# Kernel optimization log

Hardware: AMD Instinct MI355X
Metric: run time of the kernel (lower is better)

## Reference

```python
import jax, jax.numpy as jnp
import numpy as np

LAMBDA_L1 = 0.5
LAMBDA_SSIM = 0.5
ITERATIONS = 1000
THRESH = 0.01
SUB_N = 50000  # torch caps inlier-check set at 50k points


def setup_inputs() -> dict:
    key = jax.random.key(0)
    k1, k2 = jax.random.split(key)
    H, W = 1024, 2048  # Cityscapes resolution
    rendered_depth = jax.random.uniform(k1, (H, W), jnp.float32, 0.2, 10.0)
    prior_disparity = jax.random.uniform(k2, (H, W), jnp.float32, 0.0, 1.0)
    return {"rendered_depth": rendered_depth, "prior_disparity": prior_disparity}


def _ransac_linear_alignment(x, y, mask, key):
    """Fit y = s*x + t by RANSAC over masked points. x, y, mask are flat [P]."""
    P = x.shape[0]
    num_pts = mask.sum()
    # indices of masked points packed at the front (fixed-shape, jit-safe)
    idx_m = jnp.flatnonzero(mask, size=P, fill_value=0)
    k_pair, k_sub = jax.random.split(key)
    # random point pairs among the first num_pts (masked) entries
    pos = jax.random.randint(k_pair, (ITERATIONS, 2), 0, num_pts)
    pi = idx_m[pos]                                   # [iters, 2]
    x1, x2 = x[pi[:, 0]], x[pi[:, 1]]
    y1, y2 = y[pi[:, 0]], y[pi[:, 1]]
    scales = (y2 - y1) / (x2 - x1 + 1e-8)             # [iters]
    shifts = y1 - scales * x1                         # [iters]
    # subsample inlier-check set (with replacement; torch uses randperm)
    spos = jax.random.randint(k_sub, (SUB_N,), 0, num_pts)
    si = idx_m[spos]
    x_sub, y_sub = x[si], y[si]                       # [SUB_N]
    # dynamic threshold = 0.5 * MAD of masked y
    y_nan = jnp.where(mask, y, jnp.nan)
    med = jnp.nanmedian(y_nan)
    dyn = jnp.nanmedian(jnp.abs(y_nan - med)) * 0.5
    dyn = jnp.where(dyn < 1e-5, THRESH, dyn)
    # all iterations evaluated in parallel: [iters, SUB_N] residuals
    res = jnp.abs(scales[:, None] * x_sub[None, :] + shifts[:, None] - y_sub[None, :])
    counts = (res < dyn).sum(axis=1)
    counts = jnp.where(scales > 0, counts, -1)        # torch skips s <= 0
    best = jnp.argmax(counts)                         # first max == torch's strict-> update
    valid = counts[best] >= 0
    s = jnp.where(valid, scales[best], 1.0)
    t = jnp.where(valid, shifts[best], 0.0)
    # num_pts < 10 fallback
    s = jnp.where(num_pts < 10, 1.0, s)
    t = jnp.where(num_pts < 10, 0.0, t)
    return s, t


def reference(rendered_depth, prior_disparity):
    d_ren = rendered_depth
    d_pri = prior_disparity
    mask = (d_ren > 0.1) & (d_ren < 100.0) & jnp.isfinite(d_ren)
    target_inv_ren = 1.0 / (d_ren + 1e-6)
    n_valid = mask.sum()

    s, t = _ransac_linear_alignment(
        jax.lax.stop_gradient(d_pri).reshape(-1),
        jax.lax.stop_gradient(target_inv_ren).reshape(-1),
        mask.reshape(-1),
        jax.random.key(42),
    )
    aligned_prior_disp = s * d_pri + t
    # masked mean L1 (F.l1_loss over mask-selected elements)
    l1_loss = jnp.sum(jnp.abs(aligned_prior_disp - target_inv_ren) * mask) / jnp.maximum(n_valid, 1)
    total_loss = LAMBDA_L1 * l1_loss + LAMBDA_SSIM * 0.0  # ssim_module=None
    total_loss = jnp.where(n_valid < 100, 0.0, total_loss)  # early-exit branch
    prior_metric_depth = 1.0 / jnp.maximum(jax.lax.stop_gradient(aligned_prior_disp), 1e-4)
    return total_loss, target_inv_ren, prior_metric_depth
```

## Files before the change

kernel.cpp:

```cpp
#include <hip/hip_runtime.h>
#include <stdint.h>
#include <math.h>


#define NT 256
#define GA 128
#define GB 512
#define GC 128
#define GD 512
#define GE 256
#define GF 1024
#define LCAP 262144u

enum : uint32_t {
  W_CNT  = 0,
  W_LOSS = 4,
  W_N    = 6,
  W_VA   = 7, W_VB = 8,
  W_WA   = 9, W_WB = 10,
  W_SB1  = 12,
  W_SB2  = 16,
  W_COUNTS = 20,
  W_G1   = 1024,
  W_G2   = 17408,
  W_ZEND = 33792,
  W_PERC = 33792,
  W_SCALES = 34816,
  W_SHIFTS = 35816,
  W_XSUB = 36816,
  W_YSUB = 86816,
  W_LA1  = 136832,
  W_LB1  = W_LA1 + LCAP,
  W_LA2  = W_LB1 + LCAP,
  W_LB2  = W_LA2 + LCAP
};

__device__ __forceinline__ uint32_t rotl32(uint32_t v, int d) {
  return (v << d) | (v >> (32 - d));
}
__device__ __forceinline__ void tf2x32(uint32_t k0, uint32_t k1,
                                       uint32_t c0, uint32_t c1,
                                       uint32_t& o0, uint32_t& o1) {
  uint32_t ks2 = k0 ^ k1 ^ 0x1BD11BDAu;
  uint32_t x0 = c0 + k0;
  uint32_t x1 = c1 + k1;
#define TFR(r) { x0 += x1; x1 = rotl32(x1, r); x1 ^= x0; }
  TFR(13) TFR(15) TFR(26) TFR(6)
  x0 += k1;  x1 += ks2 + 1u;
  TFR(17) TFR(29) TFR(16) TFR(24)
  x0 += ks2; x1 += k0 + 2u;
  TFR(13) TFR(15) TFR(26) TFR(6)
  x0 += k0;  x1 += k1 + 3u;
  TFR(17) TFR(29) TFR(16) TFR(24)
  x0 += k1;  x1 += ks2 + 4u;
  TFR(13) TFR(15) TFR(26) TFR(6)
  x0 += ks2; x1 += k0 + 5u;
#undef TFR
  o0 = x0; o1 = x1;
}
struct Keys { uint32_t hp0, hp1, lp0, lp1, hs0, hs1, ls0, ls1; };
__device__ __forceinline__ Keys derive_keys() {
  Keys K; uint32_t p0, p1, q0, q1;
  tf2x32(0u, 42u, 0u, 0u, p0, p1);
  tf2x32(0u, 42u, 0u, 1u, q0, q1);
  tf2x32(p0, p1, 0u, 0u, K.hp0, K.hp1);
  tf2x32(p0, p1, 0u, 1u, K.lp0, K.lp1);
  tf2x32(q0, q1, 0u, 0u, K.hs0, K.hs1);
  tf2x32(q0, q1, 0u, 1u, K.ls0, K.ls1);
  return K;
}
__device__ __forceinline__ uint32_t bits32(uint32_t k0, uint32_t k1, uint32_t e) {
  uint32_t a, b; tf2x32(k0, k1, 0u, e, a, b); return a ^ b;
}
__device__ __forceinline__ uint32_t ri_offset(uint32_t hi, uint32_t lo, uint32_t span) {
  uint32_t m = 65536u % span;
  m = (m * m) % span;
  uint32_t off = (hi % span) * m + (lo % span);
  return off % span;
}

__device__ __forceinline__ uint32_t f2u(float f) {
  uint32_t u = __float_as_uint(f);
  return (u & 0x80000000u) ? ~u : (u | 0x80000000u);
}
__device__ __forceinline__ float u2f(uint32_t u) {
  uint32_t v = (u & 0x80000000u) ? (u & 0x7FFFFFFFu) : ~u;
  return __uint_as_float(v);
}
__device__ __forceinline__ uint32_t yval_u(float dv, float& y, bool& m) {
  y = __fdiv_rn(1.0f, __fadd_rn(dv, 1e-6f));
  m = (dv > 0.1f) && (dv < 100.0f) && isfinite(dv);
  return m ? f2u(y) : 0xFFFFFFFFu;
}
__device__ __forceinline__ uint32_t m2w(uint32_t u, float med) {
  return (u != 0xFFFFFFFFu) ? f2u(fabsf(__fsub_rn(u2f(u), med))) : 0xFFFFFFFFu;
}
__device__ __forceinline__ float med_from(const uint32_t* WS) {
  return __fmul_rn(__fadd_rn(u2f(WS[W_VA]), u2f(WS[W_VB])), 0.5f);
}

__device__ __forceinline__ uint32_t block_sum_u32(uint32_t v, uint32_t* wl) {
  const int lane = threadIdx.x & 63, wid = threadIdx.x >> 6;
  for (int off = 32; off > 0; off >>= 1) v += __shfl_down(v, off);
  __syncthreads();
  if (lane == 0) wl[wid] = v;
  __syncthreads();
  return wl[0] + wl[1] + wl[2] + wl[3];
}
__device__ __forceinline__ uint32_t scan_excl(uint32_t local, uint32_t* wl) {
  const int lane = threadIdx.x & 63, wid = threadIdx.x >> 6;
  __syncthreads();
  uint32_t v = local;
#pragma unroll
  for (int off = 1; off < 64; off <<= 1) {
    uint32_t o = __shfl_up(v, off);
    if (lane >= off) v += o;
  }
  if (lane == 63) wl[wid] = v;
  __syncthreads();
  uint32_t base = 0;
  for (int w = 0; w < 4; w++) if (w < wid) base += wl[w];
  return base + v - local;
}

__device__ void g_select2(const uint32_t* __restrict__ G, uint32_t rkA, uint32_t rkB,
                          uint32_t* wl, uint32_t* bc4) {
  const int tid = threadIdx.x;
  if (tid < 4) bc4[tid] = 0u;
  __syncthreads();
  uint32_t local = 0;
  for (int k = 0; k < 64; k++) local += G[tid * 64 + k];
  uint32_t excl = scan_excl(local, wl);
  for (int s = 0; s < 2; s++) {
    uint32_t rk = s ? rkB : rkA;
    if (local > 0 && rk >= excl && rk < excl + local) {
      uint32_t c = excl;
      for (int k = 0; k < 64; k++) {
        uint32_t v = G[tid * 64 + k];
        if (rk < c + v) { bc4[2 * s] = (uint32_t)(tid * 64 + k); bc4[2 * s + 1] = rk - c; break; }
        c += v;
      }
    }
  }
  __syncthreads();
}

__device__ uint32_t select17(const uint32_t* __restrict__ L, uint32_t cnt,
                             uint32_t rk, uint32_t bin14,
                             uint32_t* h512, uint32_t* h256,
                             uint32_t* wl, uint32_t* bc) {
  const int tid = threadIdx.x;
  __syncthreads();
  h512[2 * tid] = 0; h512[2 * tid + 1] = 0; h256[tid] = 0;
  if (tid < 2) bc[tid] = 0u;
  __syncthreads();
  for (uint32_t i = tid; i < cnt; i += NT)
    atomicAdd(&h512[(L[i] >> 8) & 511u], 1u);
  __syncthreads();
  uint32_t a0 = h512[2 * tid], a1 = h512[2 * tid + 1];
  uint32_t local = a0 + a1;
  uint32_t excl = scan_excl(local, wl);
  if (local > 0 && rk >= excl && rk < excl + local) {
    if (rk < excl + a0) { bc[0] = (uint32_t)(2 * tid); bc[1] = rk - excl; }
    else { bc[0] = (uint32_t)(2 * tid + 1); bc[1] = rk - excl - a0; }
  }
  __syncthreads();
  uint32_t binA = bc[0], rk2 = bc[1];
  __syncthreads();
  for (uint32_t i = tid; i < cnt; i += NT) {
    uint32_t v = L[i];
    if (((v >> 8) & 511u) == binA) atomicAdd(&h256[v & 255u], 1u);
  }
  __syncthreads();
  uint32_t l2 = h256[tid];
  uint32_t e2 = scan_excl(l2, wl);
  if (l2 > 0 && rk2 >= e2 && rk2 < e2 + l2) bc[0] = (uint32_t)tid;
  __syncthreads();
  uint32_t binB = bc[0];
  __syncthreads();
  return ((16384u + bin14) << 17) | (binA << 8) | binB;
}

__global__ void k_zero(uint32_t* WS) {
  int i = blockIdx.x * blockDim.x + threadIdx.x;
  if (i < (int)W_ZEND) WS[i] = 0u;
}

__global__ __launch_bounds__(NT) void kA(const float* __restrict__ dren,
                                         uint32_t* __restrict__ WS, int P) {
  const int tid = threadIdx.x, bid = blockIdx.x, gid = bid * NT + tid;
  __shared__ uint32_t lh[8192];
  __shared__ uint32_t wl[4];
  for (int i = tid; i < 8192; i += NT) lh[i] = 0u;
  __syncthreads();
  uint32_t cnt = 0;
  const float4* d4 = (const float4*)dren;
  const int P4 = P >> 2;
  for (int i = gid; i < P4; i += GA * NT) {
    float4 d = d4[i];
    float dc[4] = { d.x, d.y, d.z, d.w };
#pragma unroll
    for (int k = 0; k < 4; k++) {
      float y; bool m;
      uint32_t u = yval_u(dc[k], y, m);
      cnt += m ? 1u : 0u;
      uint32_t bin = (u >> 17) & 16383u;
      atomicAdd(&lh[bin >> 1], 1u << ((bin & 1u) << 4));
    }
  }
  for (int i = (P & ~3) + gid; i < P; i += GA * NT) {
    float y; bool m;
    uint32_t u = yval_u(dren[i], y, m);
    cnt += m ? 1u : 0u;
    uint32_t bin = (u >> 17) & 16383u;
    atomicAdd(&lh[bin >> 1], 1u << ((bin & 1u) << 4));
  }
  uint32_t btot = block_sum_u32(cnt, wl);
  if (tid == 0) WS[W_PERC + bid] = btot;
  __syncthreads();
  for (int w = tid; w < 8192; w += NT) {
    uint32_t pv = lh[w];
    if (pv) {
      uint32_t lo = pv & 0xFFFFu, hi = pv >> 16;
      if (lo) atomicAdd(&WS[W_G1 + 2 * w], lo);
      if (hi) atomicAdd(&WS[W_G1 + 2 * w + 1], hi);
    }
  }
}

__global__ __launch_bounds__(NT) void kB(const float* __restrict__ dren,
                                         const float* __restrict__ dpri,
                                         uint32_t* __restrict__ WS, int P) {
  const int tid = threadIdx.x, bid = blockIdx.x, gid = bid * NT + tid;
  __shared__ uint32_t bufA[4096], bufB[4096];
  __shared__ uint32_t cA, cB, baseA, baseB;
  __shared__ uint32_t wl[4], bc4[4];
  uint32_t local = (tid < GA) ? WS[W_PERC + tid] : 0u;
  const uint32_t n = block_sum_u32(local, wl);
  const uint32_t nn = n ? n : 1u;
  g_select2(WS + W_G1, (nn - 1u) >> 1, nn >> 1, wl, bc4);
  const uint32_t binA1 = bc4[0], binB1 = bc4[2];
  const bool dv1 = (binA1 != binB1);
  if (tid == 0) {
    WS[W_N] = n;
    WS[W_SB1 + 0] = bc4[0]; WS[W_SB1 + 1] = bc4[1];
    WS[W_SB1 + 2] = bc4[2]; WS[W_SB1 + 3] = bc4[3];
    cA = 0; cB = 0;
  }
  __syncthreads();
  {
    uint32_t span = n ? n : 1u;
    if (gid < 1000) {
      Keys K = derive_keys();
      uint32_t hi0 = bits32(K.hp0, K.hp1, (uint32_t)(2 * gid));
      uint32_t lo0 = bits32(K.lp0, K.lp1, (uint32_t)(2 * gid));
      uint32_t hi1 = bits32(K.hp0, K.hp1, (uint32_t)(2 * gid + 1));
      uint32_t lo1 = bits32(K.lp0, K.lp1, (uint32_t)(2 * gid + 1));
      uint32_t i0 = ri_offset(hi0, lo0, span);
      uint32_t i1 = ri_offset(hi1, lo1, span);
      float x1v = dpri[i0], x2v = dpri[i1];
      float y1v = __fdiv_rn(1.0f, __fadd_rn(dren[i0], 1e-6f));
      float y2v = __fdiv_rn(1.0f, __fadd_rn(dren[i1], 1e-6f));
      float sc = __fdiv_rn(__fsub_rn(y2v, y1v),
                           __fadd_rn(__fsub_rn(x2v, x1v), 1e-8f));
      ((float*)WS)[W_SCALES + gid] = sc;
      ((float*)WS)[W_SHIFTS + gid] = __fsub_rn(y1v, __fmul_rn(sc, x1v));
    }
    if (gid < 50000) {
      Keys K = derive_keys();
      uint32_t hi = bits32(K.hs0, K.hs1, (uint32_t)gid);
      uint32_t lo = bits32(K.ls0, K.ls1, (uint32_t)gid);
      uint32_t idx = ri_offset(hi, lo, span);
      ((float*)WS)[W_XSUB + gid] = dpri[idx];
      ((float*)WS)[W_YSUB + gid] = __fdiv_rn(1.0f, __fadd_rn(dren[idx], 1e-6f));
    }
  }
  const float4* d4 = (const float4*)dren;
  const int P4 = P >> 2;
  for (int i = gid; i < P4; i += GB * NT) {
    float4 d = d4[i];
    float dc[4] = { d.x, d.y, d.z, d.w };
#pragma unroll
    for (int k = 0; k < 4; k++) {
      float y; bool m;
      uint32_t u = yval_u(dc[k], y, m);
      uint32_t b = (u >> 17) & 16383u;
      if (b == binA1) { uint32_t j = atomicAdd(&cA, 1u); if (j < 4096u) bufA[j] = u; }
      else if (dv1 && b == binB1) { uint32_t j = atomicAdd(&cB, 1u); if (j < 4096u) bufB[j] = u; }
    }
  }
  for (int i = (P & ~3) + gid; i < P; i += GB * NT) {
    float y; bool m;
    uint32_t u = yval_u(dren[i], y, m);
    uint32_t b = (u >> 17) & 16383u;
    if (b == binA1) { uint32_t j = atomicAdd(&cA, 1u); if (j < 4096u) bufA[j] = u; }
    else if (dv1 && b == binB1) { uint32_t j = atomicAdd(&cB, 1u); if (j < 4096u) bufB[j] = u; }
  }
  __syncthreads();
  if (tid == 0) {
    uint32_t a = cA > 4096u ? 4096u : cA;
    uint32_t b = cB > 4096u ? 4096u : cB;
    cA = a; cB = b;
    baseA = a ? atomicAdd(&WS[W_CNT + 0], a) : 0u;
    baseB = b ? atomicAdd(&WS[W_CNT + 1], b) : 0u;
  }
  __syncthreads();
  for (uint32_t k = tid; k < cA; k += NT)
    if (baseA + k < LCAP) WS[W_LA1 + baseA + k] = bufA[k];
  for (uint32_t k = tid; k < cB; k += NT)
    if (baseB + k < LCAP) WS[W_LB1 + baseB + k] = bufB[k];
}

__global__ __launch_bounds__(NT) void kMed(uint32_t* __restrict__ WS) {
  const int bid = blockIdx.x;
  __shared__ uint32_t h512[512], h256[256];
  __shared__ uint32_t wl[4], bc[2];
  const uint32_t binA1 = WS[W_SB1 + 0], rkA1 = WS[W_SB1 + 1];
  const uint32_t binB1 = WS[W_SB1 + 2], rkB1 = WS[W_SB1 + 3];
  const bool dv1 = (binA1 != binB1);
  uint32_t bin, rk; const uint32_t* L; uint32_t cnt;
  if (bid == 0) {
    bin = binA1; rk = rkA1; L = WS + W_LA1;
    cnt = WS[W_CNT + 0];
  } else {
    bin = dv1 ? binB1 : binA1; rk = rkB1;
    L = dv1 ? (WS + W_LB1) : (WS + W_LA1);
    cnt = dv1 ? WS[W_CNT + 1] : WS[W_CNT + 0];
  }
  if (cnt > LCAP) cnt = LCAP;
  uint32_t v = select17(L, cnt, rk, bin, h512, h256, wl, bc);
  if (threadIdx.x == 0) WS[bid == 0 ? W_VA : W_VB] = v;
}

__global__ __launch_bounds__(NT) void kC(const float* __restrict__ dren,
                                         uint32_t* __restrict__ WS, int P) {
  const int tid = threadIdx.x, bid = blockIdx.x, gid = bid * NT + tid;
  __shared__ uint32_t lh[8192];
  const float med = med_from(WS);
  for (int i = tid; i < 8192; i += NT) lh[i] = 0u;
  __syncthreads();
  const float4* d4 = (const float4*)dren;
  const int P4 = P >> 2;
  for (int i = gid; i < P4; i += GC * NT) {
    float4 d = d4[i];
    float dc[4] = { d.x, d.y, d.z, d.w };
#pragma unroll
    for (int k = 0; k < 4; k++) {
      float y; bool m;
      uint32_t w = m2w(yval_u(dc[k], y, m), med);
      uint32_t bin = (w >> 17) & 16383u;
      atomicAdd(&lh[bin >> 1], 1u << ((bin & 1u) << 4));
    }
  }
  for (int i = (P & ~3) + gid; i < P; i += GC * NT) {
    float y; bool m;
    uint32_t w = m2w(yval_u(dren[i], y, m), med);
    uint32_t bin = (w >> 17) & 16383u;
    atomicAdd(&lh[bin >> 1], 1u << ((bin & 1u) << 4));
  }
  __syncthreads();
  for (int w = tid; w < 8192; w += NT) {
    uint32_t pv = lh[w];
    if (pv) {
      uint32_t lo = pv & 0xFFFFu, hi = pv >> 16;
      if (lo) atomicAdd(&WS[W_G2 + 2 * w], lo);
      if (hi) atomicAdd(&WS[W_G2 + 2 * w + 1], hi);
    }
  }
}

__global__ __launch_bounds__(NT) void kD(const float* __restrict__ dren,
                                         uint32_t* __restrict__ WS, int P) {
  const int tid = threadIdx.x, bid = blockIdx.x, gid = bid * NT + tid;
  __shared__ uint32_t bufA[4096], bufB[4096];
  __shared__ uint32_t cA, cB, baseA, baseB;
  __shared__ uint32_t wl[4], bc4[4];
  const float med = med_from(WS);
  const uint32_t n = WS[W_N];
  const uint32_t nn = n ? n : 1u;
  g_select2(WS + W_G2, (nn - 1u) >> 1, nn >> 1, wl, bc4);
  const uint32_t binA2 = bc4[0], binB2 = bc4[2];
  const bool dv2 = (binA2 != binB2);
  if (tid == 0) {
    WS[W_SB2 + 0] = bc4[0]; WS[W_SB2 + 1] = bc4[1];
    WS[W_SB2 + 2] = bc4[2]; WS[W_SB2 + 3] = bc4[3];
    cA = 0; cB = 0;
  }
  __syncthreads();
  const float4* d4 = (const float4*)dren;
  const int P4 = P >> 2;
  for (int i = gid; i < P4; i += GD * NT) {
    float4 d = d4[i];
    float dc[4] = { d.x, d.y, d.z, d.w };
#pragma unroll
    for (int k = 0; k < 4; k++) {
      float y; bool m;
      uint32_t w = m2w(yval_u(dc[k], y, m), med);
      uint32_t b = (w >> 17) & 16383u;
      if (b == binA2) { uint32_t j = atomicAdd(&cA, 1u); if (j < 4096u) bufA[j] = w; }
      else if (dv2 && b == binB2) { uint32_t j = atomicAdd(&cB, 1u); if (j < 4096u) bufB[j] = w; }
    }
  }
  for (int i = (P & ~3) + gid; i < P; i += GD * NT) {
    float y; bool m;
    uint32_t w = m2w(yval_u(dren[i], y, m), med);
    uint32_t b = (w >> 17) & 16383u;
    if (b == binA2) { uint32_t j = atomicAdd(&cA, 1u); if (j < 4096u) bufA[j] = w; }
    else if (dv2 && b == binB2) { uint32_t j = atomicAdd(&cB, 1u); if (j < 4096u) bufB[j] = w; }
  }
  __syncthreads();
  if (tid == 0) {
    uint32_t a = cA > 4096u ? 4096u : cA;
    uint32_t b = cB > 4096u ? 4096u : cB;
    cA = a; cB = b;
    baseA = a ? atomicAdd(&WS[W_CNT + 2], a) : 0u;
    baseB = b ? atomicAdd(&WS[W_CNT + 3], b) : 0u;
  }
  __syncthreads();
  for (uint32_t k = tid; k < cA; k += NT)
    if (baseA + k < LCAP) WS[W_LA2 + baseA + k] = bufA[k];
  for (uint32_t k = tid; k < cB; k += NT)
    if (baseB + k < LCAP) WS[W_LB2 + baseB + k] = bufB[k];
}

__global__ __launch_bounds__(NT) void kDyn(uint32_t* __restrict__ WS) {
  const int bid = blockIdx.x;
  __shared__ uint32_t h512[512], h256[256];
  __shared__ uint32_t wl[4], bc[2];
  const uint32_t binA2 = WS[W_SB2 + 0], rkA2 = WS[W_SB2 + 1];
  const uint32_t binB2 = WS[W_SB2 + 2], rkB2 = WS[W_SB2 + 3];
  const bool dv2 = (binA2 != binB2);
  uint32_t bin, rk; const uint32_t* L; uint32_t cnt;
  if (bid == 0) {
    bin = binA2; rk = rkA2; L = WS + W_LA2;
    cnt = WS[W_CNT + 2];
  } else {
    bin = dv2 ? binB2 : binA2; rk = rkB2;
    L = dv2 ? (WS + W_LB2) : (WS + W_LA2);
    cnt = dv2 ? WS[W_CNT + 3] : WS[W_CNT + 2];
  }
  if (cnt > LCAP) cnt = LCAP;
  uint32_t v = select17(L, cnt, rk, bin, h512, h256, wl, bc);
  if (threadIdx.x == 0) WS[bid == 0 ? W_WA : W_WB] = v;
}

__global__ __launch_bounds__(NT) void kE(uint32_t* __restrict__ WS) {
  const int tid = threadIdx.x, bid = blockIdx.x;
  __shared__ float lx[200], ly[200];
  float mad = __fmul_rn(__fadd_rn(u2f(WS[W_WA]), u2f(WS[W_WB])), 0.5f);
  float dyn = __fmul_rn(mad, 0.5f);
  if (dyn < 1e-5f) dyn = 0.01f;
  const int e0 = (bid * 50000) / GE, e1 = ((bid + 1) * 50000) / GE;
  const int cnt = e1 - e0;
  const float* x_sub = (const float*)WS + W_XSUB;
  const float* y_sub = (const float*)WS + W_YSUB;
  if (tid < cnt) { lx[tid] = x_sub[e0 + tid]; ly[tid] = y_sub[e0 + tid]; }
  __syncthreads();
  const float* scales = (const float*)WS + W_SCALES;
  const float* shifts = (const float*)WS + W_SHIFTS;
  float ss[4], tt[4]; int c[4];
#pragma unroll
  for (int j = 0; j < 4; j++) {
    int cand = tid + 256 * j;
    ss[j] = (cand < 1000) ? scales[cand] : 0.0f;
    tt[j] = (cand < 1000) ? shifts[cand] : 0.0f;
    c[j] = 0;
  }
  for (int e = 0; e < cnt; e++) {
    float xe = lx[e], ye = ly[e];
#pragma unroll
    for (int j = 0; j < 4; j++) {
      float r = fabsf(__fsub_rn(__fadd_rn(__fmul_rn(ss[j], xe), tt[j]), ye));
      c[j] += (r < dyn) ? 1 : 0;
    }
  }
  int* counts = (int*)WS + W_COUNTS;
#pragma unroll
  for (int j = 0; j < 4; j++) {
    int cand = tid + 256 * j;
    if (cand < 1000 && c[j] > 0) atomicAdd(&counts[cand], c[j]);
  }
}

__global__ __launch_bounds__(NT) void kF(const float* __restrict__ dren,
                                         const float* __restrict__ dpri,
                                         float* __restrict__ out,
                                         uint32_t* __restrict__ WS, int P) {
  const int tid = threadIdx.x, bid = blockIdx.x, gid = bid * NT + tid;
  const int lane = tid & 63, wid = tid >> 6;
  __shared__ int ired[4], iidx[4];
  __shared__ float fbcast[2];
  __shared__ double dred[4];
  {
    const int* counts = (const int*)WS + W_COUNTS;
    const float* scales = (const float*)WS + W_SCALES;
    const float* shifts = (const float*)WS + W_SHIFTS;
    int bcn = -2, bix = 0x7FFFFFFF;
    for (int j = tid; j < 1000; j += NT) {
      int cc = counts[j];
      if (!(scales[j] > 0.0f)) cc = -1;
      if (cc > bcn) { bcn = cc; bix = j; }
    }
    for (int off = 32; off > 0; off >>= 1) {
      int oc = __shfl_down(bcn, off), oi = __shfl_down(bix, off);
      if (oc > bcn || (oc == bcn && oi < bix)) { bcn = oc; bix = oi; }
    }
    if (lane == 0) { ired[wid] = bcn; iidx[wid] = bix; }
    __syncthreads();
    if (tid == 0) {
      for (int w = 1; w < 4; w++) {
        if (ired[w] > ired[0] || (ired[w] == ired[0] && iidx[w] < iidx[0])) {
          ired[0] = ired[w]; iidx[0] = iidx[w];
        }
      }
      bool valid = ired[0] >= 0;
      float s = valid ? scales[iidx[0]] : 1.0f;
      float t = valid ? shifts[iidx[0]] : 0.0f;
      uint32_t n = WS[W_N];
      if (n < 10u) { s = 1.0f; t = 0.0f; }
      fbcast[0] = s; fbcast[1] = t;
    }
    __syncthreads();
  }
  const float s = fbcast[0], t = fbcast[1];
  float* out_y = out + 1;
  float* out_depth = out + 1 + P;
  double acc = 0.0;
  const float4* d4 = (const float4*)dren;
  const float4* p4 = (const float4*)dpri;
  const int P4 = P >> 2;
  for (int i = gid; i < P4; i += GF * NT) {
    float4 d = d4[i], p = p4[i];
    float dc[4] = { d.x, d.y, d.z, d.w };
    float pc[4] = { p.x, p.y, p.z, p.w };
#pragma unroll
    for (int k = 0; k < 4; k++) {
      float yv = __fdiv_rn(1.0f, __fadd_rn(dc[k], 1e-6f));
      out_y[4 * i + k] = yv;
      float al = __fadd_rn(__fmul_rn(s, pc[k]), t);
      out_depth[4 * i + k] = __fdiv_rn(1.0f, fmaxf(al, 1e-4f));
      bool m = (dc[k] > 0.1f) && (dc[k] < 100.0f) && isfinite(dc[k]);
      if (m) acc += (double)fabsf(__fsub_rn(al, yv));
    }
  }
  for (int i = (P & ~3) + gid; i < P; i += GF * NT) {
    float dv = dren[i];
    float yv = __fdiv_rn(1.0f, __fadd_rn(dv, 1e-6f));
    out_y[i] = yv;
    float al = __fadd_rn(__fmul_rn(s, dpri[i]), t);
    out_depth[i] = __fdiv_rn(1.0f, fmaxf(al, 1e-4f));
    bool m = (dv > 0.1f) && (dv < 100.0f) && isfinite(dv);
    if (m) acc += (double)fabsf(__fsub_rn(al, yv));
  }
  for (int off = 32; off > 0; off >>= 1) acc += __shfl_down(acc, off);
  __syncthreads();
  if (lane == 0) dred[wid] = acc;
  __syncthreads();
  if (tid == 0)
    atomicAdd((double*)(WS + W_LOSS), dred[0] + dred[1] + dred[2] + dred[3]);
}

__global__ void kG(const uint32_t* __restrict__ WS, float* __restrict__ out) {
  if (threadIdx.x == 0 && blockIdx.x == 0) {
    double total = *((const double*)(WS + W_LOSS));
    uint32_t n = WS[W_N];
    uint32_t nd = n ? n : 1u;
    float l1 = __fdiv_rn((float)total, (float)nd);
    out[0] = (n < 100u) ? 0.0f : __fmul_rn(0.5f, l1);
  }
}

extern "C" void kernel_launch(void* const* d_in, const int* in_sizes, int n_in,
                              void* d_out, int out_size, void* d_ws, size_t ws_size,
                              hipStream_t stream) {
  const float* d_ren = (const float*)d_in[0];
  const float* d_pri = (const float*)d_in[1];
  float* out = (float*)d_out;
  uint32_t* WS = (uint32_t*)d_ws;
  int P = in_sizes[0];

  k_zero<<<(W_ZEND + NT - 1) / NT, NT, 0, stream>>>(WS);
  kA<<<GA, NT, 0, stream>>>(d_ren, WS, P);
  kB<<<GB, NT, 0, stream>>>(d_ren, d_pri, WS, P);
  kMed<<<2, NT, 0, stream>>>(WS);
  kC<<<GC, NT, 0, stream>>>(d_ren, WS, P);
  kD<<<GD, NT, 0, stream>>>(d_ren, WS, P);
  kDyn<<<2, NT, 0, stream>>>(WS);
  kE<<<GE, NT, 0, stream>>>(WS);
  kF<<<GF, NT, 0, stream>>>(d_ren, d_pri, out, WS, P);
  kG<<<1, 64, 0, stream>>>(WS, out);
}
```

Measured before the change: 226.2 us.

## Build fine median histograms during compaction to shrink single-block select kernels

Measured after the change: 197.5 us. 1.14x faster.

```diff
diff --git a/kernel.cpp b/kernel.cpp
--- a/kernel.cpp
+++ b/kernel.cpp
@@ -23,13 +23,17 @@
   W_COUNTS = 20,
   W_G1   = 1024,
   W_G2   = 17408,
-  W_ZEND = 33792,
-  W_PERC = 33792,
-  W_SCALES = 34816,
-  W_SHIFTS = 35816,
-  W_XSUB = 36816,
-  W_YSUB = 86816,
-  W_LA1  = 136832,
+  W_H1A  = 33792,
+  W_H1B  = 35840,
+  W_H2A  = 37888,
+  W_H2B  = 39936,
+  W_ZEND = 41984,
+  W_PERC = 41984,
+  W_SCALES = 43008,
+  W_SHIFTS = 44008,
+  W_XSUB = 45008,
+  W_YSUB = 95008,
+  W_LA1  = 145024,
   W_LB1  = W_LA1 + LCAP,
   W_LA2  = W_LB1 + LCAP,
   W_LB2  = W_LA2 + LCAP
@@ -145,40 +149,25 @@
   __syncthreads();
 }
 
-__device__ uint32_t select17(const uint32_t* __restrict__ L, uint32_t cnt,
-                             uint32_t rk, uint32_t bin14,
-                             uint32_t* h512, uint32_t* h256,
-                             uint32_t* wl, uint32_t* bc) {
+__device__ void h_select(const uint32_t* __restrict__ H, uint32_t rk,
+                         uint32_t* wl, uint32_t* bc) {
   const int tid = threadIdx.x;
-  __syncthreads();
-  h512[2 * tid] = 0; h512[2 * tid + 1] = 0; h256[tid] = 0;
   if (tid < 2) bc[tid] = 0u;
   __syncthreads();
-  for (uint32_t i = tid; i < cnt; i += NT)
-    atomicAdd(&h512[(L[i] >> 8) & 511u], 1u);
-  __syncthreads();
-  uint32_t a0 = h512[2 * tid], a1 = h512[2 * tid + 1];
-  uint32_t local = a0 + a1;
+  uint32_t v8[8];
+  uint32_t local = 0;
+#pragma unroll
+  for (int k = 0; k < 8; k++) { v8[k] = H[tid * 8 + k]; local += v8[k]; }
   uint32_t excl = scan_excl(local, wl);
   if (local > 0 && rk >= excl && rk < excl + local) {
-    if (rk < excl + a0) { bc[0] = (uint32_t)(2 * tid); bc[1] = rk - excl; }
-    else { bc[0] = (uint32_t)(2 * tid + 1); bc[1] = rk - excl - a0; }
-  }
-  __syncthreads();
-  uint32_t binA = bc[0], rk2 = bc[1];
-  __syncthreads();
-  for (uint32_t i = tid; i < cnt; i += NT) {
-    uint32_t v = L[i];
-    if (((v >> 8) & 511u) == binA) atomicAdd(&h256[v & 255u], 1u);
-  }
-  __syncthreads();
-  uint32_t l2 = h256[tid];
-  uint32_t e2 = scan_excl(l2, wl);
-  if (l2 > 0 && rk2 >= e2 && rk2 < e2 + l2) bc[0] = (uint32_t)tid;
-  __syncthreads();
-  uint32_t binB = bc[0];
-  __syncthreads();
-  return ((16384u + bin14) << 17) | (binA << 8) | binB;
+    uint32_t c = excl;
+#pragma unroll
+    for (int k = 0; k < 8; k++) {
+      if (rk < c + v8[k]) { bc[0] = (uint32_t)(tid * 8 + k); bc[1] = rk - c; break; }
+      c += v8[k];
+    }
+  }
+  __syncthreads();
 }
 
 __global__ void k_zero(uint32_t* WS) {
@@ -233,6 +222,7 @@
                                          uint32_t* __restrict__ WS, int P) {
   const int tid = threadIdx.x, bid = blockIdx.x, gid = bid * NT + tid;
   __shared__ uint32_t bufA[4096], bufB[4096];
+  __shared__ uint32_t h2A[2048], h2B[2048];
   __shared__ uint32_t cA, cB, baseA, baseB;
   __shared__ uint32_t wl[4], bc4[4];
   uint32_t local = (tid < GA) ? WS[W_PERC + tid] : 0u;
@@ -247,6 +237,7 @@
     WS[W_SB1 + 2] = bc4[2]; WS[W_SB1 + 3] = bc4[3];
     cA = 0; cB = 0;
   }
+  for (int i = tid; i < 2048; i += NT) { h2A[i] = 0u; h2B[i] = 0u; }
   __syncthreads();
   {
     uint32_t span = n ? n : 1u;
@@ -285,16 +276,26 @@
       float y; bool m;
       uint32_t u = yval_u(dc[k], y, m);
       uint32_t b = (u >> 17) & 16383u;
-      if (b == binA1) { uint32_t j = atomicAdd(&cA, 1u); if (j < 4096u) bufA[j] = u; }
-      else if (dv1 && b == binB1) { uint32_t j = atomicAdd(&cB, 1u); if (j < 4096u) bufB[j] = u; }
+      if (b == binA1) {
+        uint32_t j = atomicAdd(&cA, 1u); if (j < 4096u) bufA[j] = u;
+        atomicAdd(&h2A[(u >> 6) & 2047u], 1u);
+      } else if (dv1 && b == binB1) {
+        uint32_t j = atomicAdd(&cB, 1u); if (j < 4096u) bufB[j] = u;
+        atomicAdd(&h2B[(u >> 6) & 2047u], 1u);
+      }
     }
   }
   for (int i = (P & ~3) + gid; i < P; i += GB * NT) {
     float y; bool m;
     uint32_t u = yval_u(dren[i], y, m);
     uint32_t b = (u >> 17) & 16383u;
-    if (b == binA1) { uint32_t j = atomicAdd(&cA, 1u); if (j < 4096u) bufA[j] = u; }
-    else if (dv1 && b == binB1) { uint32_t j = atomicAdd(&cB, 1u); if (j < 4096u) bufB[j] = u; }
+    if (b == binA1) {
+      uint32_t j = atomicAdd(&cA, 1u); if (j < 4096u) bufA[j] = u;
+      atomicAdd(&h2A[(u >> 6) & 2047u], 1u);
+    } else if (dv1 && b == binB1) {
+      uint32_t j = atomicAdd(&cB, 1u); if (j < 4096u) bufB[j] = u;
+      atomicAdd(&h2B[(u >> 6) & 2047u], 1u);
+    }
   }
   __syncthreads();
   if (tid == 0) {
@@ -309,27 +310,69 @@
     if (baseA + k < LCAP) WS[W_LA1 + baseA + k] = bufA[k];
   for (uint32_t k = tid; k < cB; k += NT)
     if (baseB + k < LCAP) WS[W_LB1 + baseB + k] = bufB[k];
+  for (int w = tid; w < 2048; w += NT) {
+    uint32_t a = h2A[w]; if (a) atomicAdd(&WS[W_H1A + w], a);
+    uint32_t b = h2B[w]; if (b) atomicAdd(&WS[W_H1B + w], b);
+  }
 }
 
 __global__ __launch_bounds__(NT) void kMed(uint32_t* __restrict__ WS) {
-  const int bid = blockIdx.x;
-  __shared__ uint32_t h512[512], h256[256];
+  const int tid = threadIdx.x, bid = blockIdx.x;
+  __shared__ uint32_t tiny[256];
+  __shared__ uint32_t h64[64];
   __shared__ uint32_t wl[4], bc[2];
+  __shared__ uint32_t tcnt;
   const uint32_t binA1 = WS[W_SB1 + 0], rkA1 = WS[W_SB1 + 1];
   const uint32_t binB1 = WS[W_SB1 + 2], rkB1 = WS[W_SB1 + 3];
   const bool dv1 = (binA1 != binB1);
-  uint32_t bin, rk; const uint32_t* L; uint32_t cnt;
+  uint32_t coarse, rk; const uint32_t *L, *H; uint32_t cnt;
   if (bid == 0) {
-    bin = binA1; rk = rkA1; L = WS + W_LA1;
+    coarse = binA1; rk = rkA1; L = WS + W_LA1; H = WS + W_H1A;
     cnt = WS[W_CNT + 0];
   } else {
-    bin = dv1 ? binB1 : binA1; rk = rkB1;
+    coarse = dv1 ? binB1 : binA1; rk = rkB1;
     L = dv1 ? (WS + W_LB1) : (WS + W_LA1);
+    H = dv1 ? (WS + W_H1B) : (WS + W_H1A);
     cnt = dv1 ? WS[W_CNT + 1] : WS[W_CNT + 0];
   }
   if (cnt > LCAP) cnt = LCAP;
-  uint32_t v = select17(L, cnt, rk, bin, h512, h256, wl, bc);
-  if (threadIdx.x == 0) WS[bid == 0 ? W_VA : W_VB] = v;
+  h_select(H, rk, wl, bc);
+  const uint32_t bin11 = bc[0], rk2 = bc[1];
+  if (tid == 0) tcnt = 0u;
+  if (tid < 64) h64[tid] = 0u;
+  if (tid < 2) { __syncthreads(); } else { __syncthreads(); }
+  {
+    uint32_t i = (uint32_t)tid;
+    while (i + 7u * NT < cnt) {
+      uint32_t v[8];
+#pragma unroll
+      for (int k = 0; k < 8; k++) v[k] = L[i + (uint32_t)k * NT];
+#pragma unroll
+      for (int k = 0; k < 8; k++)
+        if (((v[k] >> 6) & 2047u) == bin11) {
+          uint32_t j = atomicAdd(&tcnt, 1u); if (j < 256u) tiny[j] = v[k];
+        }
+      i += 8u * NT;
+    }
+    for (; i < cnt; i += NT) {
+      uint32_t v = L[i];
+      if (((v >> 6) & 2047u) == bin11) {
+        uint32_t j = atomicAdd(&tcnt, 1u); if (j < 256u) tiny[j] = v;
+      }
+    }
+  }
+  __syncthreads();
+  uint32_t m = tcnt; if (m > 256u) m = 256u;
+  for (uint32_t i = tid; i < m; i += NT) atomicAdd(&h64[tiny[i] & 63u], 1u);
+  __syncthreads();
+  if (tid < 2) bc[tid] = 0u;
+  uint32_t local = (tid < 64) ? h64[tid] : 0u;
+  uint32_t excl = scan_excl(local, wl);
+  if (local > 0 && rk2 >= excl && rk2 < excl + local) bc[0] = (uint32_t)tid;
+  __syncthreads();
+  const uint32_t bin6 = bc[0];
+  if (tid == 0)
+    WS[bid == 0 ? W_VA : W_VB] = ((16384u + coarse) << 17) | (bin11 << 6) | bin6;
 }
 
 __global__ __launch_bounds__(NT) void kC(const float* __restrict__ dren,
@@ -373,6 +416,7 @@
                                          uint32_t* __restrict__ WS, int P) {
   const int tid = threadIdx.x, bid = blockIdx.x, gid = bid * NT + tid;
   __shared__ uint32_t bufA[4096], bufB[4096];
+  __shared__ uint32_t h2A[2048], h2B[2048];
   __shared__ uint32_t cA, cB, baseA, baseB;
   __shared__ uint32_t wl[4], bc4[4];
   const float med = med_from(WS);
@@ -386,6 +430,7 @@
     WS[W_SB2 + 2] = bc4[2]; WS[W_SB2 + 3] = bc4[3];
     cA = 0; cB = 0;
   }
+  for (int i = tid; i < 2048; i += NT) { h2A[i] = 0u; h2B[i] = 0u; }
   __syncthreads();
   const float4* d4 = (const float4*)dren;
   const int P4 = P >> 2;
@@ -397,16 +442,26 @@
       float y; bool m;
       uint32_t w = m2w(yval_u(dc[k], y, m), med);
       uint32_t b = (w >> 17) & 16383u;
-      if (b == binA2) { uint32_t j = atomicAdd(&cA, 1u); if (j < 4096u) bufA[j] = w; }
-      else if (dv2 && b == binB2) { uint32_t j = atomicAdd(&cB, 1u); if (j < 4096u) bufB[j] = w; }
+      if (b == binA2) {
+        uint32_t j = atomicAdd(&cA, 1u); if (j < 4096u) bufA[j] = w;
+        atomicAdd(&h2A[(w >> 6) & 2047u], 1u);
+      } else if (dv2 && b == binB2) {
+        uint32_t j = atomicAdd(&cB, 1u); if (j < 4096u) bufB[j] = w;
+        atomicAdd(&h2B[(w >> 6) & 2047u], 1u);
+      }
     }
   }
   for (int i = (P & ~3) + gid; i < P; i += GD * NT) {
     float y; bool m;
     uint32_t w = m2w(yval_u(dren[i], y, m), med);
     uint32_t b = (w >> 17) & 16383u;
-    if (b == binA2) { uint32_t j = atomicAdd(&cA, 1u); if (j < 4096u) bufA[j] = w; }
-    else if (dv2 && b == binB2) { uint32_t j = atomicAdd(&cB, 1u); if (j < 4096u) bufB[j] = w; }
+    if (b == binA2) {
+      uint32_t j = atomicAdd(&cA, 1u); if (j < 4096u) bufA[j] = w;
+      atomicAdd(&h2A[(w >> 6) & 2047u], 1u);
+    } else if (dv2 && b == binB2) {
+      uint32_t j = atomicAdd(&cB, 1u); if (j < 4096u) bufB[j] = w;
+      atomicAdd(&h2B[(w >> 6) & 2047u], 1u);
+    }
   }
   __syncthreads();
   if (tid == 0) {
@@ -421,27 +476,69 @@
     if (baseA + k < LCAP) WS[W_LA2 + baseA + k] = bufA[k];
   for (uint32_t k = tid; k < cB; k += NT)
     if (baseB + k < LCAP) WS[W_LB2 + baseB + k] = bufB[k];
+  for (int w = tid; w < 2048; w += NT) {
+    uint32_t a = h2A[w]; if (a) atomicAdd(&WS[W_H2A + w], a);
+    uint32_t b = h2B[w]; if (b) atomicAdd(&WS[W_H2B + w], b);
+  }
 }
 
 __global__ __launch_bounds__(NT) void kDyn(uint32_t* __restrict__ WS) {
-  const int bid = blockIdx.x;
-  __shared__ uint32_t h512[512], h256[256];
+  const int tid = threadIdx.x, bid = blockIdx.x;
+  __shared__ uint32_t tiny[256];
+  __shared__ uint32_t h64[64];
   __shared__ uint32_t wl[4], bc[2];
+  __shared__ uint32_t tcnt;
   const uint32_t binA2 = WS[W_SB2 + 0], rkA2 = WS[W_SB2 + 1];
   const uint32_t binB2 = WS[W_SB2 + 2], rkB2 = WS[W_SB2 + 3];
   const bool dv2 = (binA2 != binB2);
-  uint32_t bin, rk; const uint32_t* L; uint32_t cnt;
+  uint32_t coarse, rk; const uint32_t *L, *H; uint32_t cnt;
   if (bid == 0) {
-    bin = binA2; rk = rkA2; L = WS + W_LA2;
+    coarse = binA2; rk = rkA2; L = WS + W_LA2; H = WS + W_H2A;
     cnt = WS[W_CNT + 2];
   } else {
-    bin = dv2 ? binB2 : binA2; rk = rkB2;
+    coarse = dv2 ? binB2 : binA2; rk = rkB2;
     L = dv2 ? (WS + W_LB2) : (WS + W_LA2);
+    H = dv2 ? (WS + W_H2B) : (WS + W_H2A);
     cnt = dv2 ? WS[W_CNT + 3] : WS[W_CNT + 2];
   }
   if (cnt > LCAP) cnt = LCAP;
-  uint32_t v = select17(L, cnt, rk, bin, h512, h256, wl, bc);
-  if (threadIdx.x == 0) WS[bid == 0 ? W_WA : W_WB] = v;
+  h_select(H, rk, wl, bc);
+  const uint32_t bin11 = bc[0], rk2 = bc[1];
+  if (tid == 0) tcnt = 0u;
+  if (tid < 64) h64[tid] = 0u;
+  __syncthreads();
+  {
+    uint32_t i = (uint32_t)tid;
+    while (i + 7u * NT < cnt) {
+      uint32_t v[8];
+#pragma unroll
+      for (int k = 0; k < 8; k++) v[k] = L[i + (uint32_t)k * NT];
+#pragma unroll
+      for (int k = 0; k < 8; k++)
+        if (((v[k] >> 6) & 2047u) == bin11) {
+          uint32_t j = atomicAdd(&tcnt, 1u); if (j < 256u) tiny[j] = v[k];
+        }
+      i += 8u * NT;
+    }
+    for (; i < cnt; i += NT) {
+      uint32_t v = L[i];
+      if (((v >> 6) & 2047u) == bin11) {
+        uint32_t j = atomicAdd(&tcnt, 1u); if (j < 256u) tiny[j] = v;
+      }
+    }
+  }
+  __syncthreads();
+  uint32_t m = tcnt; if (m > 256u) m = 256u;
+  for (uint32_t i = tid; i < m; i += NT) atomicAdd(&h64[tiny[i] & 63u], 1u);
+  __syncthreads();
+  if (tid < 2) bc[tid] = 0u;
+  uint32_t local = (tid < 64) ? h64[tid] : 0u;
+  uint32_t excl = scan_excl(local, wl);
+  if (local > 0 && rk2 >= excl && rk2 < excl + local) bc[0] = (uint32_t)tid;
+  __syncthreads();
+  const uint32_t bin6 = bc[0];
+  if (tid == 0)
+    WS[bid == 0 ? W_WA : W_WB] = ((16384u + coarse) << 17) | (bin11 << 6) | bin6;
 }
 
 __global__ __launch_bounds__(NT) void kE(uint32_t* __restrict__ WS) {
```
